# Kernel optimization log

Measured on AMD Instinct MI355X. Metric: run time of the kernel, lower is better.

The kernel has to match this reference:

```python
import jax, jax.numpy as jnp
import numpy as np
import math

B, T, EMB, HD = 4, 2048, 2048, 128
HALF = HD // 2


def setup_inputs() -> dict:
    key = jax.random.key(0)
    ks = jax.random.split(key, 4)
    x = jax.random.normal(ks[0], (B, T, EMB), dtype=jnp.float32)
    s = 1.0 / math.sqrt(EMB)
    Wq = jax.random.normal(ks[1], (EMB, HD), dtype=jnp.float32) * s
    Wk = jax.random.normal(ks[2], (EMB, HD), dtype=jnp.float32) * s
    Wv = jax.random.normal(ks[3], (EMB, HD), dtype=jnp.float32) * s
    # Standard RoPE rotation table: theta_i = 10000^(-2i/HD), angle = pos * theta
    inv_freq = 1.0 / (10000.0 ** (np.arange(0, HALF, dtype=np.float32) / HALF))
    angles = np.arange(T, dtype=np.float32)[:, None] * inv_freq[None, :]  # [T, HALF]
    rot_cos = jnp.asarray(np.cos(angles), dtype=jnp.float32)
    rot_sin = jnp.asarray(np.sin(angles), dtype=jnp.float32)
    # Additive causal mask: 0 on/below diagonal, -1e9 above
    NEG = -1e9
    mask = jnp.where(jnp.tril(jnp.ones((T, T), dtype=bool)), 0.0, NEG).astype(jnp.float32)
    return {"x": x, "Wq": Wq, "Wk": Wk, "Wv": Wv,
            "rot_cos": rot_cos, "rot_sin": rot_sin, "mask": mask}


def _apply_rope(q, rot_cos, rot_sin):
    # q: [B, T, HD]; view last dim as HALF complex pairs and rotate
    qp = q.reshape(q.shape[0], q.shape[1], HALF, 2)
    re, im = qp[..., 0], qp[..., 1]
    out_re = re * rot_cos - im * rot_sin  # broadcast [T,HALF] over batch
    out_im = re * rot_sin + im * rot_cos
    return jnp.stack([out_re, out_im], axis=-1).reshape(q.shape)


def reference(x, Wq, Wk, Wv, rot_cos, rot_sin, mask):
    Q = x @ Wq  # [B, T, HD]
    K = x @ Wk
    V = x @ Wv
    Q = _apply_rope(Q, rot_cos, rot_sin)
    K = _apply_rope(K, rot_cos, rot_sin)
    scores = jnp.einsum('bqd,bkd->bqk', Q, K) / math.sqrt(HD)
    probs = jax.nn.softmax(scores + mask, axis=-1)  # dropout is identity in eval
    return jnp.einsum('bqk,bkd->bqd', probs, V)
```

## Files before the change

kernel.cpp:

```cpp
#include <hip/hip_runtime.h>
#include <cstddef>
#include <cstdint>

#define T_SEQ 2048
#define EMB_D 2048
#define HD_D  128

typedef __attribute__((ext_vector_type(8))) short short8;
typedef __attribute__((ext_vector_type(4))) float f32x4;
typedef __attribute__((ext_vector_type(4))) unsigned short ushort4v;
typedef __attribute__((ext_vector_type(8))) unsigned short ushort8v;

union frag_u { short8 s8; unsigned u[4]; };

static __device__ __forceinline__ unsigned short f2bf_rne(float f) {
    union { float f; unsigned u; } v; v.f = f;
    unsigned r = v.u + 0x7fffu + ((v.u >> 16) & 1u);
    return (unsigned short)(r >> 16);
}
static __device__ __forceinline__ unsigned short f2bf_fast(float f) {
    union { float f; unsigned u; } v; v.f = f;
    return (unsigned short)((v.u + 0x8000u) >> 16);
}
static __device__ __forceinline__ float bf2f(unsigned short h) {
    union { unsigned u; float f; } v; v.u = ((unsigned)h) << 16;
    return v.f;
}
static __device__ __forceinline__ unsigned pk2(float a, float b) {
    union { float f; unsigned u; } x, y; x.f = a; y.f = b;
    return __builtin_amdgcn_perm(y.u + 0x8000u, x.u + 0x8000u, 0x07060302);
}
static __device__ __forceinline__ void dma16(const void* g, void* l) {
    __builtin_amdgcn_global_load_lds(
        (const __attribute__((address_space(1))) unsigned int*)g,
        (__attribute__((address_space(3))) unsigned int*)l, 16, 0, 0);
}
#define EXP2F(x) __builtin_amdgcn_exp2f(x)

__global__ __launch_bounds__(256) void prep_weights(
    const float* __restrict__ Wq, const float* __restrict__ Wk,
    const float* __restrict__ Wv, unsigned short* __restrict__ Wt)
{
    __shared__ __attribute__((aligned(16))) unsigned short tw[64 * 132];
    const int w = blockIdx.y;
    const int k0 = blockIdx.x * 64;
    const float* W = (w == 0) ? Wq : (w == 1) ? Wk : Wv;
    const int tid = threadIdx.x;
#pragma unroll
    for (int p = 0; p < 8; p++) {
        const int f = p * 256 + tid;
        const int row = f >> 5, c4 = f & 31;
        const float4 v = *(const float4*)&W[(size_t)(k0 + row) * HD_D + c4 * 4];
        ushort4v h = { f2bf_rne(v.x), f2bf_rne(v.y), f2bf_rne(v.z), f2bf_rne(v.w) };
        *(ushort4v*)&tw[row * 132 + c4 * 4] = h;
    }
    __syncthreads();
    const int kk = (tid & 7) * 8;
#pragma unroll
    for (int p = 0; p < 4; p++) {
        const int n = p * 32 + (tid >> 3);
        ushort8v o;
#pragma unroll
        for (int jj = 0; jj < 8; jj++) o[jj] = tw[(kk + jj) * 132 + n];
        *(ushort8v*)&Wt[(size_t)w * (HD_D * EMB_D) + (size_t)n * EMB_D + k0 + kk] = o;
    }
}

__global__ __launch_bounds__(256, 4) void qkv_fused(
    const float* __restrict__ x, const unsigned short* __restrict__ Wt,
    const float* __restrict__ rcos, const float* __restrict__ rsin,
    unsigned short* __restrict__ Qb, unsigned short* __restrict__ Kb,
    unsigned short* __restrict__ Vt)
{
    __shared__ __attribute__((aligned(16))) float xs[2][32 * 64];
    __shared__ __attribute__((aligned(16))) unsigned short wsb[2][96 * 64];
    const int L = blockIdx.x;
    const int xcd = L & 7, s = L >> 3;
    const int ng = s & 3;
    const int m0 = (xcd * 32 + (s >> 2)) * 32;
    const int tid = threadIdx.x;
    const int lane = tid & 63, wave = tid >> 6;
    const int wm = wave >> 1, wn = wave & 1;
    const int l15 = lane & 15, lq = lane >> 4;

    const float* xSrc[2]; int xOff[2];
#pragma unroll
    for (int p = 0; p < 2; p++) {
        const int g = p * 256 + tid;
        const int row = g >> 4, c = g & 15;
        xSrc[p] = x + (size_t)(m0 + row) * EMB_D + (c ^ (row & 15)) * 4;
        xOff[p] = (p * 256 + wave * 64) * 4;
    }
    const unsigned short* wgSrc[3]; int wgSlot[3];
#pragma unroll
    for (int p = 0; p < 3; p++) {
        const int g = p * 256 + tid;
        const int row = g >> 3, c = g & 7;
        wgSrc[p] = Wt + (size_t)(ng * 96 + row) * EMB_D + c * 8;
        wgSlot[p] = row * 64 + (c ^ (row & 7)) * 8;
    }

    int offA[2][2];
#pragma unroll
    for (int ks = 0; ks < 2; ks++) {
        const int row = wm * 16 + l15;
        const int ga = ks * 8 + lq * 2;
        offA[ks][0] = row * 64 + ((ga)     ^ (row & 15)) * 4;
        offA[ks][1] = row * 64 + ((ga + 1) ^ (row & 15)) * 4;
    }
    int offB[3][2];
#pragma unroll
    for (int j = 0; j < 3; j++)
#pragma unroll
        for (int ks = 0; ks < 2; ks++) {
            const int row = wn * 48 + j * 16 + l15;
            const int gb = ks * 4 + lq;
            offB[j][ks] = row * 64 + (gb ^ (row & 7)) * 8;
        }

    f32x4 acc[3];
#pragma unroll
    for (int j = 0; j < 3; j++) acc[j] = (f32x4){0.f, 0.f, 0.f, 0.f};

    {
        short8 wreg[3];
#pragma unroll
        for (int p = 0; p < 3; p++) wreg[p] = *(const short8*)(wgSrc[p]);
#pragma unroll
        for (int p = 0; p < 2; p++) dma16(xSrc[p], &xs[0][xOff[p]]);
#pragma unroll
        for (int p = 0; p < 3; p++) *(short8*)&wsb[0][wgSlot[p]] = wreg[p];
    }

    for (int k0 = 0; k0 < EMB_D; k0 += 64) {
        const int buf = (k0 >> 6) & 1;
        const bool more = (k0 + 64) < EMB_D;
        __syncthreads();

        short8 wreg[3];
        if (more) {
#pragma unroll
            for (int p = 0; p < 3; p++)
                wreg[p] = *(const short8*)(wgSrc[p] + k0 + 64);
#pragma unroll
            for (int p = 0; p < 2; p++)
                dma16(xSrc[p] + k0 + 64, &xs[buf ^ 1][xOff[p]]);
        }

        frag_u A[2];
#pragma unroll
        for (int ks = 0; ks < 2; ks++) {
            const f32x4 f0 = *(const f32x4*)&xs[buf][offA[ks][0]];
            const f32x4 f1 = *(const f32x4*)&xs[buf][offA[ks][1]];
            A[ks].u[0] = pk2(f0.x, f0.y);
            A[ks].u[1] = pk2(f0.z, f0.w);
            A[ks].u[2] = pk2(f1.x, f1.y);
            A[ks].u[3] = pk2(f1.z, f1.w);
        }
#pragma unroll
        for (int ks = 0; ks < 2; ks++)
#pragma unroll
            for (int j = 0; j < 3; j++) {
                const short8 B = *(const short8*)&wsb[buf][offB[j][ks]];
                acc[j] = __builtin_amdgcn_mfma_f32_16x16x32_bf16(
                    A[ks].s8, B, acc[j], 0, 0, 0);
            }

        if (more) {
#pragma unroll
            for (int p = 0; p < 3; p++)
                *(short8*)&wsb[buf ^ 1][wgSlot[p]] = wreg[p];
        }
    }

    const float qscale = 0.08838834764831845f * 1.4426950408889634f;
#pragma unroll
    for (int r = 0; r < 4; r++) {
        const int row = m0 + wm * 16 + lq * 4 + r;
        const int t = row & (T_SEQ - 1);
        const int bb = row >> 11;
#pragma unroll
        for (int j = 0; j < 3; j++) {
            const int col = ng * 96 + wn * 48 + j * 16 + l15;
            const int mat = col >> 7, mcol = col & 127;
            const float v = acc[j][r];
            if (mat == 2) {
                Vt[((size_t)bb * HD_D + mcol) * T_SEQ + t] = f2bf_rne(v);
            } else {
                const int ip = mcol >> 1;
                const float c = rcos[t * 64 + ip];
                const float s2 = rsin[t * 64 + ip];
                const float pv = __shfl_xor(v, 1);
                float rv = (mcol & 1) ? (pv * s2 + v * c) : (v * c - pv * s2);
                if (mat == 0) {
                    rv *= qscale;
                    Qb[(size_t)row * HD_D + mcol] = f2bf_rne(rv);
                } else {
                    Kb[(size_t)row * HD_D + mcol] = f2bf_rne(rv);
                }
            }
        }
    }
}

__global__ __launch_bounds__(256, 2) void attn(
    const unsigned short* __restrict__ Qb, const unsigned short* __restrict__ Kb,
    const unsigned short* __restrict__ Vt, float* __restrict__ O0,
    unsigned short* __restrict__ O1, float* __restrict__ Lp)
{
    __shared__ __attribute__((aligned(16))) unsigned short O_s[4][16 * 128];
    __shared__ __attribute__((aligned(16))) unsigned short P_s[4][2][16 * 40];
    __shared__ float l_s[4][16];

    const int tid = threadIdx.x;
    const int lane = tid & 63, wave = tid >> 6;
    const int l15 = lane & 15, lq = lane >> 4;
    const int kf = lq * 8;

    const int L = blockIdx.x;
    const int g = L & 1;
    const int b = (L >> 1) & 3;
    const int q0 = (127 - (L >> 3)) * 16;
    const int kend = q0 + 16;
    const float M2 = 16.0f;

    const unsigned short* Qp = Qb + (size_t)(b * T_SEQ + q0) * HD_D;
    short8 aQ[4];
#pragma unroll
    for (int d = 0; d < 4; d++)
        aQ[d] = *(const short8*)&Qp[l15 * HD_D + d * 32 + kf];

    f32x4 acc[8];
#pragma unroll
    for (int d = 0; d < 8; d++) acc[d] = (f32x4){0.f, 0.f, 0.f, 0.f};
    float l_r[4] = {0.f, 0.f, 0.f, 0.f};

    const unsigned short* Kbase = Kb + (size_t)b * T_SEQ * HD_D;
    const unsigned short* Vbase = Vt + (size_t)b * HD_D * T_SEQ;
    unsigned short* PwA = &P_s[wave][0][0];
    unsigned short* PwB = &P_s[wave][1][0];

    for (int c = 2 * wave + g; c * 32 < kend; c += 16) {
        const int kA = c * 32;
        const int kB = (c + 8) * 32;
        const bool hB = kB < kend;

        const unsigned short* KpA = Kbase + (size_t)kA * HD_D;
        const unsigned short* KpB = Kbase + (size_t)kB * HD_D;
        short8 KA[8], KB_[8];
#pragma unroll
        for (int d = 0; d < 4; d++)
#pragma unroll
            for (int n = 0; n < 2; n++)
                KA[d * 2 + n] = *(const short8*)&KpA[(size_t)(n * 16 + l15) * HD_D + d * 32 + kf];
        if (hB) {
#pragma unroll
            for (int d = 0; d < 4; d++)
#pragma unroll
                for (int n = 0; n < 2; n++)
                    KB_[d * 2 + n] = *(const short8*)&KpB[(size_t)(n * 16 + l15) * HD_D + d * 32 + kf];
        }

        f32x4 sA0 = (f32x4){0.f, 0.f, 0.f, 0.f}, sA1 = sA0, sB0 = sA0, sB1 = sA0;
#pragma unroll
        for (int d = 0; d < 4; d++) {
            sA0 = __builtin_amdgcn_mfma_f32_16x16x32_bf16(aQ[d], KA[d * 2 + 0], sA0, 0, 0, 0);
            sA1 = __builtin_amdgcn_mfma_f32_16x16x32_bf16(aQ[d], KA[d * 2 + 1], sA1, 0, 0, 0);
        }
        if (hB) {
#pragma unroll
            for (int d = 0; d < 4; d++) {
                sB0 = __builtin_amdgcn_mfma_f32_16x16x32_bf16(aQ[d], KB_[d * 2 + 0], sB0, 0, 0, 0);
                sB1 = __builtin_amdgcn_mfma_f32_16x16x32_bf16(aQ[d], KB_[d * 2 + 1], sB1, 0, 0, 0);
            }
        }

        short8 VA[8];
#pragma unroll
        for (int d = 0; d < 8; d++)
            VA[d] = *(const short8*)&Vbase[(size_t)(d * 16 + l15) * T_SEQ + kA + kf];

#pragma unroll
        for (int r = 0; r < 4; r++) {
            const int q = q0 + lq * 4 + r;
            const float p0 = ((kA + l15)      <= q) ? EXP2F(sA0[r] - M2) : 0.f;
            const float p1 = ((kA + 16 + l15) <= q) ? EXP2F(sA1[r] - M2) : 0.f;
            l_r[r] += p0 + p1;
            const int prow = (lq * 4 + r) * 40;
            PwA[prow + l15]      = f2bf_fast(p0);
            PwA[prow + 16 + l15] = f2bf_fast(p1);
        }
        const short8 pA = *(const short8*)&PwA[l15 * 40 + kf];
#pragma unroll
        for (int d = 0; d < 8; d++)
            acc[d] = __builtin_amdgcn_mfma_f32_16x16x32_bf16(pA, VA[d], acc[d], 0, 0, 0);

        if (hB) {
            short8 VB[8];
#pragma unroll
            for (int d = 0; d < 8; d++)
                VB[d] = *(const short8*)&Vbase[(size_t)(d * 16 + l15) * T_SEQ + kB + kf];
#pragma unroll
            for (int r = 0; r < 4; r++) {
                const int q = q0 + lq * 4 + r;
                const float p0 = ((kB + l15)      <= q) ? EXP2F(sB0[r] - M2) : 0.f;
                const float p1 = ((kB + 16 + l15) <= q) ? EXP2F(sB1[r] - M2) : 0.f;
                l_r[r] += p0 + p1;
                const int prow = (lq * 4 + r) * 40;
                PwB[prow + l15]      = f2bf_fast(p0);
                PwB[prow + 16 + l15] = f2bf_fast(p1);
            }
            const short8 pB = *(const short8*)&PwB[l15 * 40 + kf];
#pragma unroll
            for (int d = 0; d < 8; d++)
                acc[d] = __builtin_amdgcn_mfma_f32_16x16x32_bf16(pB, VB[d], acc[d], 0, 0, 0);
        }
    }

#pragma unroll
    for (int r = 0; r < 4; r++) {
        float lr = l_r[r];
        lr += __shfl_xor(lr, 1);
        lr += __shfl_xor(lr, 2);
        lr += __shfl_xor(lr, 4);
        lr += __shfl_xor(lr, 8);
        if (l15 == 0) l_s[wave][lq * 4 + r] = lr;
#pragma unroll
        for (int d = 0; d < 8; d++)
            O_s[wave][(lq * 4 + r) * 128 + d * 16 + l15] = f2bf_fast(acc[d][r]);
    }
    __syncthreads();

    const int row = tid >> 4;
    const int dc = (tid & 15) * 8;
    const float lt = l_s[0][row] + l_s[1][row] + l_s[2][row] + l_s[3][row];
    float o[8];
#pragma unroll
    for (int k = 0; k < 8; k++) o[k] = 0.f;
#pragma unroll
    for (int w2 = 0; w2 < 4; w2++) {
        const ushort8v pv = *(const ushort8v*)&O_s[w2][row * 128 + dc];
#pragma unroll
        for (int k = 0; k < 8; k++) o[k] += bf2f(pv[k]);
    }
    const size_t grow = (size_t)(b * T_SEQ + q0 + row);
    if (g == 0) {
        float* op = O0 + grow * HD_D + dc;
#pragma unroll
        for (int k = 0; k < 8; k++) op[k] = o[k];
    } else {
        ushort8v h;
#pragma unroll
        for (int k = 0; k < 8; k++) h[k] = f2bf_fast(o[k]);
        *(ushort8v*)&O1[grow * HD_D + dc] = h;
    }
    if ((tid & 15) == 0) Lp[g * 8192 + grow] = lt;
}

__global__ __launch_bounds__(256) void attn_merge(
    float* __restrict__ out, const unsigned short* __restrict__ O1,
    const float* __restrict__ Lp)
{
    const int idx = blockIdx.x * 256 + threadIdx.x;
    const int row = idx >> 5;
    f32x4 a = ((f32x4*)out)[idx];
    const ushort4v h = ((const ushort4v*)O1)[idx];
    f32x4 bv = { bf2f(h.x), bf2f(h.y), bf2f(h.z), bf2f(h.w) };
    const float inv = 1.0f / (Lp[row] + Lp[8192 + row]);
    ((f32x4*)out)[idx] = (a + bv) * inv;
}

extern "C" void kernel_launch(void* const* d_in, const int* in_sizes, int n_in,
                              void* d_out, int out_size, void* d_ws, size_t ws_size,
                              hipStream_t stream)
{
    (void)in_sizes; (void)n_in; (void)out_size; (void)ws_size;
    const float* x  = (const float*)d_in[0];
    const float* Wq = (const float*)d_in[1];
    const float* Wk = (const float*)d_in[2];
    const float* Wv = (const float*)d_in[3];
    const float* rc = (const float*)d_in[4];
    const float* rs = (const float*)d_in[5];
    float* out = (float*)d_out;

    char* ws = (char*)d_ws;
    unsigned short* Wt = (unsigned short*)(ws);
    unsigned short* Qb = (unsigned short*)(ws + 1572864);
    unsigned short* Kb = (unsigned short*)(ws + 3670016);
    unsigned short* Vt = (unsigned short*)(ws + 5767168);
    unsigned short* O1 = (unsigned short*)(ws + 7864320);
    float*          Lp = (float*)(ws + 9961472);

    prep_weights<<<dim3(32, 3), 256, 0, stream>>>(Wq, Wk, Wv, Wt);
    qkv_fused   <<<dim3(1024),  256, 0, stream>>>(x, Wt, rc, rs, Qb, Kb, Vt);
    attn        <<<dim3(1024),  256, 0, stream>>>(Qb, Kb, Vt, out, O1, Lp);
    attn_merge  <<<dim3(1024),  256, 0, stream>>>(out, O1, Lp);
}
```

Baseline: 190.0 us.

## Fuse split-K attention merge into attn via atomic last-block counter

Removes the separate attn_merge kernel launch. Each pair of key-split blocks for a query tile now increments an atomic counter, and the second block to finish reads the partner's partial output and row sum and writes the normalized result. Counters are zeroed in prep_weights. This saves a kernel launch plus a full extra pass over the output, at the cost of a threadfence, an atomic per block and some serialization in the finishing block.

```diff
diff --git a/kernel.cpp b/kernel.cpp
--- a/kernel.cpp
+++ b/kernel.cpp
@@ -39,13 +39,18 @@
 
 __global__ __launch_bounds__(256) void prep_weights(
     const float* __restrict__ Wq, const float* __restrict__ Wk,
-    const float* __restrict__ Wv, unsigned short* __restrict__ Wt)
+    const float* __restrict__ Wv, unsigned short* __restrict__ Wt,
+    int* __restrict__ cnt)
 {
     __shared__ __attribute__((aligned(16))) unsigned short tw[64 * 132];
     const int w = blockIdx.y;
     const int k0 = blockIdx.x * 64;
     const float* W = (w == 0) ? Wq : (w == 1) ? Wk : Wv;
     const int tid = threadIdx.x;
+    if (blockIdx.x == 0 && w == 0) {
+        cnt[tid] = 0;
+        cnt[256 + tid] = 0;
+    }
 #pragma unroll
     for (int p = 0; p < 8; p++) {
         const int f = p * 256 + tid;
@@ -206,11 +211,13 @@
 __global__ __launch_bounds__(256, 2) void attn(
     const unsigned short* __restrict__ Qb, const unsigned short* __restrict__ Kb,
     const unsigned short* __restrict__ Vt, float* __restrict__ O0,
-    unsigned short* __restrict__ O1, float* __restrict__ Lp)
+    unsigned short* __restrict__ O1, float* __restrict__ Lp,
+    int* __restrict__ cnt)
 {
     __shared__ __attribute__((aligned(16))) unsigned short O_s[4][16 * 128];
     __shared__ __attribute__((aligned(16))) unsigned short P_s[4][2][16 * 40];
     __shared__ float l_s[4][16];
+    __shared__ int last_s;
 
     const int tid = threadIdx.x;
     const int lane = tid & 63, wave = tid >> 6;
@@ -221,6 +228,7 @@
     const int g = L & 1;
     const int b = (L >> 1) & 3;
     const int q0 = (127 - (L >> 3)) * 16;
+    const int qidx = L >> 1;
     const int kend = q0 + 16;
     const float M2 = 16.0f;
 
@@ -344,6 +352,7 @@
         for (int k = 0; k < 8; k++) o[k] += bf2f(pv[k]);
     }
     const size_t grow = (size_t)(b * T_SEQ + q0 + row);
+
     if (g == 0) {
         float* op = O0 + grow * HD_D + dc;
 #pragma unroll
@@ -355,19 +364,46 @@
         *(ushort8v*)&O1[grow * HD_D + dc] = h;
     }
     if ((tid & 15) == 0) Lp[g * 8192 + grow] = lt;
-}
-
-__global__ __launch_bounds__(256) void attn_merge(
-    float* __restrict__ out, const unsigned short* __restrict__ O1,
-    const float* __restrict__ Lp)
-{
-    const int idx = blockIdx.x * 256 + threadIdx.x;
-    const int row = idx >> 5;
-    f32x4 a = ((f32x4*)out)[idx];
-    const ushort4v h = ((const ushort4v*)O1)[idx];
-    f32x4 bv = { bf2f(h.x), bf2f(h.y), bf2f(h.z), bf2f(h.w) };
-    const float inv = 1.0f / (Lp[row] + Lp[8192 + row]);
-    ((f32x4*)out)[idx] = (a + bv) * inv;
+
+    __threadfence();
+    __syncthreads();
+    if (tid == 0) {
+        last_s = __hip_atomic_fetch_add(&cnt[qidx], 1, __ATOMIC_ACQ_REL,
+                                        __HIP_MEMORY_SCOPE_AGENT);
+    }
+    __syncthreads();
+    if (last_s == 1) {
+        const float ltp = __hip_atomic_load(&Lp[(g ^ 1) * 8192 + grow],
+                                            __ATOMIC_RELAXED, __HIP_MEMORY_SCOPE_AGENT);
+        const float inv = 1.0f / (lt + ltp);
+        float po[8];
+        if (g == 1) {
+            const unsigned long long* pp =
+                (const unsigned long long*)(O0 + grow * HD_D + dc);
+#pragma unroll
+            for (int k = 0; k < 4; k++) {
+                union { unsigned long long u; float f[2]; } cv;
+                cv.u = __hip_atomic_load(pp + k, __ATOMIC_RELAXED,
+                                         __HIP_MEMORY_SCOPE_AGENT);
+                po[2 * k]     = cv.f[0];
+                po[2 * k + 1] = cv.f[1];
+            }
+        } else {
+            const unsigned long long* pp =
+                (const unsigned long long*)(O1 + grow * HD_D + dc);
+#pragma unroll
+            for (int k = 0; k < 2; k++) {
+                union { unsigned long long u; unsigned short h[4]; } cv;
+                cv.u = __hip_atomic_load(pp + k, __ATOMIC_RELAXED,
+                                         __HIP_MEMORY_SCOPE_AGENT);
+#pragma unroll
+                for (int j = 0; j < 4; j++) po[4 * k + j] = bf2f(cv.h[j]);
+            }
+        }
+        float* op = O0 + grow * HD_D + dc;
+#pragma unroll
+        for (int k = 0; k < 8; k++) op[k] = (o[k] + po[k]) * inv;
+    }
 }
 
 extern "C" void kernel_launch(void* const* d_in, const int* in_sizes, int n_in,
@@ -390,9 +426,9 @@
     unsigned short* Vt = (unsigned short*)(ws + 5767168);
     unsigned short* O1 = (unsigned short*)(ws + 7864320);
     float*          Lp = (float*)(ws + 9961472);
-
-    prep_weights<<<dim3(32, 3), 256, 0, stream>>>(Wq, Wk, Wv, Wt);
+    int*            cnt = (int*)(ws + 10027008);
+
+    prep_weights<<<dim3(32, 3), 256, 0, stream>>>(Wq, Wk, Wv, Wt, cnt);
     qkv_fused   <<<dim3(1024),  256, 0, stream>>>(x, Wt, rc, rs, Qb, Kb, Vt);
-    attn        <<<dim3(1024),  256, 0, stream>>>(Qb, Kb, Vt, out, O1, Lp);
-    attn_merge  <<<dim3(1024),  256, 0, stream>>>(out, O1, Lp);
-}
+    attn        <<<dim3(1024),  256, 0, stream>>>(Qb, Kb, Vt, out, O1, Lp, cnt);
+}
```

After: 363.9 us. 1.92x slower.
